# Optimization experiments

Measured on AMD Instinct MI355X. Metric: run time of the kernel, lower is better.

The kernel has to match this reference:

```python
import jax, jax.numpy as jnp
import numpy as np
from jax import lax

B, T, IN, H, OUT = 4096, 512, 2, 12, 2


def setup_inputs() -> dict:
    key = jax.random.key(0)
    ks = jax.random.split(key, 11)
    s = 1.0 / np.sqrt(H)  # PyTorch LSTM init scale
    f32 = jnp.float32
    return {
        "x": jax.random.normal(ks[0], (B, T, IN), dtype=f32),
        "W_ih0": jax.random.uniform(ks[1], (4 * H, IN), dtype=f32, minval=-s, maxval=s),
        "W_hh0": jax.random.uniform(ks[2], (4 * H, H), dtype=f32, minval=-s, maxval=s),
        "b_ih0": jax.random.uniform(ks[3], (4 * H,), dtype=f32, minval=-s, maxval=s),
        "b_hh0": jax.random.uniform(ks[4], (4 * H,), dtype=f32, minval=-s, maxval=s),
        "W_ih1": jax.random.uniform(ks[5], (4 * H, H), dtype=f32, minval=-s, maxval=s),
        "W_hh1": jax.random.uniform(ks[6], (4 * H, H), dtype=f32, minval=-s, maxval=s),
        "b_ih1": jax.random.uniform(ks[7], (4 * H,), dtype=f32, minval=-s, maxval=s),
        "b_hh1": jax.random.uniform(ks[8], (4 * H,), dtype=f32, minval=-s, maxval=s),
        "fc_W": jax.random.uniform(ks[9], (OUT, H), dtype=f32, minval=-s, maxval=s),
        "fc_b": jax.random.uniform(ks[10], (OUT,), dtype=f32, minval=-s, maxval=s),
    }


def _lstm_layer(x, W_ih, W_hh, b_ih, b_hh):
    # x: [B, T, in_dim] -> hidden trajectory [B, T, H]
    b, h = x.shape[0], W_hh.shape[1]
    # Precompute input contribution for all timesteps: [T, B, 4H]
    xg = jnp.einsum('bti,gi->tbg', x, W_ih) + b_ih + b_hh

    def step(carry, xg_t):
        hprev, cprev = carry
        gates = xg_t + hprev @ W_hh.T  # [B, 4H], PyTorch gate order i,f,g,o
        i, f, g, o = jnp.split(gates, 4, axis=-1)
        i = jax.nn.sigmoid(i)
        f = jax.nn.sigmoid(f)
        g = jnp.tanh(g)
        o = jax.nn.sigmoid(o)
        c = f * cprev + i * g
        hnew = o * jnp.tanh(c)
        return (hnew, c), hnew

    z = jnp.zeros((b, h), dtype=x.dtype)
    _, hs = lax.scan(step, (z, z), xg)  # hs: [T, B, H]
    return jnp.swapaxes(hs, 0, 1)  # [B, T, H]


def reference(x, W_ih0, W_hh0, b_ih0, b_hh0, W_ih1, W_hh1, b_ih1, b_hh1, fc_W, fc_b):
    # 2-layer LSTM, h0=c0=0; dropout is identity in eval mode.
    h1 = _lstm_layer(x, W_ih0, W_hh0, b_ih0, b_hh0)   # [B, T, H]
    h2 = _lstm_layer(h1, W_ih1, W_hh1, b_ih1, b_hh1)  # [B, T, H]
    last = h2[:, -1, :]                               # [B, H]
    return last @ fc_W.T + fc_b                       # [B, OUT]
```

## Files before the change

### kernel.cpp

```cpp
#include <hip/hip_runtime.h>


namespace {
constexpr int H  = 12;
constexpr int T  = 512;
constexpr int IN = 2;
constexpr float LOG2E = 1.4426950408889634f;

typedef float f2 __attribute__((ext_vector_type(2)));

__device__ __forceinline__ f2 pk_fma(f2 a, f2 b, f2 c) {
    f2 d;
    asm("v_pk_fma_f32 %0, %1, %2, %3" : "=v"(d) : "v"(a), "v"(b), "v"(c));
    return d;
}
__device__ __forceinline__ float exp2_(float x) {
    float r;
    asm("v_exp_f32 %0, %1" : "=v"(r) : "v"(x));
    return r;
}
__device__ __forceinline__ float rcp_(float x) { return __builtin_amdgcn_rcpf(x); }

template <int CTRL>
__device__ __forceinline__ float dppf(float v) {
    return __int_as_float(__builtin_amdgcn_update_dpp(
        __float_as_int(v), __float_as_int(v), CTRL, 0xF, 0xF, true));
}
constexpr int QP1 = 0x39;
constexpr int QP2 = 0x4E;
constexpr int QP3 = 0x93;

__device__ __forceinline__ float tanh_(float c) {
    return fmaf(2.0f, rcp_(1.0f + exp2_(-2.0f * LOG2E * c)), -1.0f);
}
}

__global__ __launch_bounds__(256, 4) void lstm2_fc_kernel(
    const float* __restrict__ x,
    const float* __restrict__ W_ih0,
    const float* __restrict__ W_hh0,
    const float* __restrict__ b_ih0,
    const float* __restrict__ b_hh0,
    const float* __restrict__ W_ih1,
    const float* __restrict__ W_hh1,
    const float* __restrict__ b_ih1,
    const float* __restrict__ b_hh1,
    const float* __restrict__ fc_W,
    const float* __restrict__ fc_b,
    float* __restrict__ out)
{
    const int lane = threadIdx.x & 63;
    const int wid  = __builtin_amdgcn_readfirstlane((int)threadIdx.x >> 6);
    const int b    = blockIdx.x * 4 + wid;
    const int u    = lane >> 2;
    const int gate = lane & 3;
    const int uc   = (u < H) ? u : 0;
    const int r    = gate * H + uc;

    const float pre  = (gate == 2) ? 2.0f : 1.0f;
    const float kmul = -LOG2E * pre;
    const float pa   = 1.0f - pre;

    __shared__ __align__(16) float sm[4 * 2 * 96];
    const int base0 = wid * 192;
    const int base1 = base0 + 96;
    const bool writer = (gate == 0) && (u < H);
    const int  woff   = writer ? uc : (16 + lane);
    const int  wslot0 = base0 + woff;
    const int  wslot1 = base1 + woff;

    f2 wx, whh0p[6], wih1p[6], whh1p[6];
    wx.x = kmul * W_ih0[r * IN + 0];
    wx.y = kmul * W_ih0[r * IN + 1];
#pragma unroll
    for (int k = 0; k < 6; ++k) {
        whh0p[k].x = kmul * W_hh0[r * H + 2 * k];
        whh0p[k].y = kmul * W_hh0[r * H + 2 * k + 1];
        wih1p[k].x = kmul * W_ih1[r * H + 2 * k];
        wih1p[k].y = kmul * W_ih1[r * H + 2 * k + 1];
        whh1p[k].x = kmul * W_hh1[r * H + 2 * k];
        whh1p[k].y = kmul * W_hh1[r * H + 2 * k + 1];
    }
    f2 bias0p, bias1p;
    bias0p.x = kmul * (b_ih0[r] + b_hh0[r]); bias0p.y = 0.0f;
    bias1p.x = kmul * (b_ih1[r] + b_hh1[r]); bias1p.y = 0.0f;

    float c0 = 0.0f, c1 = 0.0f;
    f2 hp0[6], hq1[6];
#pragma unroll
    for (int k = 0; k < 6; ++k) { hp0[k] = (f2)(0.0f); hq1[k] = (f2)(0.0f); }

    const float* xp = x + (size_t)b * T * IN;
    f2 xv; xv.x = xp[0]; xv.y = xp[1];

    for (int t = 0; t < T; ++t) {
        const int tn = (t < T - 1) ? (t + 1) : t;
        f2 xn; xn.x = xp[2 * tn + 0]; xn.y = xp[2 * tn + 1];

        f2 acc = pk_fma(wx, xv, bias0p);
#pragma unroll
        for (int k = 0; k < 6; ++k) acc = pk_fma(whh0p[k], hp0[k], acc);
        const float s0 = fmaf(pre, rcp_(1.0f + exp2_(acc.x + acc.y)), pa);
        const float f0 = dppf<QP1>(s0);
        const float g0 = dppf<QP2>(s0);
        const float o0 = dppf<QP3>(s0);
        c0 = fmaf(f0, c0, s0 * g0);
        const float h0v = o0 * tanh_(c0);
        sm[wslot0] = h0v;

        f2 accC = pk_fma(whh1p[0], hq1[0], bias1p);
#pragma unroll
        for (int k = 1; k < 6; ++k) accC = pk_fma(whh1p[k], hq1[k], accC);
#pragma unroll
        for (int k = 0; k < 6; ++k) hp0[k] = *(const f2*)&sm[base0 + 2 * k];
#pragma unroll
        for (int k = 0; k < 6; ++k) accC = pk_fma(wih1p[k], hp0[k], accC);
        const float s1 = fmaf(pre, rcp_(1.0f + exp2_(accC.x + accC.y)), pa);
        const float f1 = dppf<QP1>(s1);
        const float g1 = dppf<QP2>(s1);
        const float o1 = dppf<QP3>(s1);
        c1 = fmaf(f1, c1, s1 * g1);
        const float h1v = o1 * tanh_(c1);
        sm[wslot1] = h1v;
#pragma unroll
        for (int k = 0; k < 6; ++k) hq1[k] = *(const f2*)&sm[base1 + 2 * k];

        xv = xn;
    }

    if (lane == 0) {
        float r0 = fc_b[0];
        float r1 = fc_b[1];
#pragma unroll
        for (int k = 0; k < 6; ++k) {
            r0 = fmaf(fc_W[2 * k], hq1[k].x, r0);
            r0 = fmaf(fc_W[2 * k + 1], hq1[k].y, r0);
            r1 = fmaf(fc_W[H + 2 * k], hq1[k].x, r1);
            r1 = fmaf(fc_W[H + 2 * k + 1], hq1[k].y, r1);
        }
        float2 res; res.x = r0; res.y = r1;
        *(float2*)(out + (size_t)b * 2) = res;
    }
}

extern "C" void kernel_launch(void* const* d_in, const int* in_sizes, int n_in,
                              void* d_out, int out_size, void* d_ws, size_t ws_size,
                              hipStream_t stream) {
    const float* x     = (const float*)d_in[0];
    const float* W_ih0 = (const float*)d_in[1];
    const float* W_hh0 = (const float*)d_in[2];
    const float* b_ih0 = (const float*)d_in[3];
    const float* b_hh0 = (const float*)d_in[4];
    const float* W_ih1 = (const float*)d_in[5];
    const float* W_hh1 = (const float*)d_in[6];
    const float* b_ih1 = (const float*)d_in[7];
    const float* b_hh1 = (const float*)d_in[8];
    const float* fc_W  = (const float*)d_in[9];
    const float* fc_b  = (const float*)d_in[10];
    float* out = (float*)d_out;

    lstm2_fc_kernel<<<1024, 256, 0, stream>>>(
        x, W_ih0, W_hh0, b_ih0, b_hh0,
        W_ih1, W_hh1, b_ih1, b_hh1, fc_W, fc_b, out);
}
```

Before: 258.0 us.

## Split LSTM dot-product chains, unroll timesteps by two, load x as float4

Each gate dot product now uses three independent packed-FMA accumulators that are summed at the end, instead of one serial FMA chain. This shortens the dependency latency on the recurrent critical path. Timesteps are processed in pairs, and the two x inputs are fetched together as one float4 load. Shared-memory writes are predicated to only the writer lanes, replacing the dummy-slot trick, and compiler memory fences are added, which rely on wave-level LDS ordering for correctness.

```diff
diff --git a/kernel.cpp b/kernel.cpp
--- a/kernel.cpp
+++ b/kernel.cpp
@@ -4,22 +4,26 @@
 namespace {
 constexpr int H  = 12;
 constexpr int T  = 512;
-constexpr int IN = 2;
 constexpr float LOG2E = 1.4426950408889634f;
 
 typedef float f2 __attribute__((ext_vector_type(2)));
+typedef float f4 __attribute__((ext_vector_type(4)));
 
-__device__ __forceinline__ f2 pk_fma(f2 a, f2 b, f2 c) {
-    f2 d;
-    asm("v_pk_fma_f32 %0, %1, %2, %3" : "=v"(d) : "v"(a), "v"(b), "v"(c));
-    return d;
+__device__ __forceinline__ f2 pkfma(f2 a, f2 b, f2 c) {
+    asm("v_pk_fma_f32 %0, %1, %2, %0" : "+v"(c) : "v"(a), "v"(b));
+    return c;
+}
+__device__ __forceinline__ f2 pkmul(f2 a, f2 b) {
+    f2 d; asm("v_pk_mul_f32 %0, %1, %2" : "=v"(d) : "v"(a), "v"(b)); return d;
+}
+__device__ __forceinline__ f2 pkadd(f2 a, f2 b) {
+    f2 d; asm("v_pk_add_f32 %0, %1, %2" : "=v"(d) : "v"(a), "v"(b)); return d;
 }
 __device__ __forceinline__ float exp2_(float x) {
-    float r;
-    asm("v_exp_f32 %0, %1" : "=v"(r) : "v"(x));
-    return r;
+    float r; asm("v_exp_f32 %0, %1" : "=v"(r) : "v"(x)); return r;
 }
 __device__ __forceinline__ float rcp_(float x) { return __builtin_amdgcn_rcpf(x); }
+__device__ __forceinline__ void memfence_() { asm volatile("" ::: "memory"); }
 
 template <int CTRL>
 __device__ __forceinline__ float dppf(float v) {
@@ -29,10 +33,6 @@
 constexpr int QP1 = 0x39;
 constexpr int QP2 = 0x4E;
 constexpr int QP3 = 0x93;
-
-__device__ __forceinline__ float tanh_(float c) {
-    return fmaf(2.0f, rcp_(1.0f + exp2_(-2.0f * LOG2E * c)), -1.0f);
-}
 }
 
 __global__ __launch_bounds__(256, 4) void lstm2_fc_kernel(
@@ -60,18 +60,17 @@
     const float pre  = (gate == 2) ? 2.0f : 1.0f;
     const float kmul = -LOG2E * pre;
     const float pa   = 1.0f - pre;
+    const float km2  = -2.0f * LOG2E;
 
-    __shared__ __align__(16) float sm[4 * 2 * 96];
-    const int base0 = wid * 192;
-    const int base1 = base0 + 96;
+    __shared__ __align__(16) float sm[4 * 32];
+    float* smb = &sm[wid * 32];
     const bool writer = (gate == 0) && (u < H);
-    const int  woff   = writer ? uc : (16 + lane);
-    const int  wslot0 = base0 + woff;
-    const int  wslot1 = base1 + woff;
+    float* smw0 = smb + uc;
+    float* smw1 = smb + 16 + uc;
 
     f2 wx, whh0p[6], wih1p[6], whh1p[6];
-    wx.x = kmul * W_ih0[r * IN + 0];
-    wx.y = kmul * W_ih0[r * IN + 1];
+    wx.x = kmul * W_ih0[r * 2 + 0];
+    wx.y = kmul * W_ih0[r * 2 + 1];
 #pragma unroll
     for (int k = 0; k < 6; ++k) {
         whh0p[k].x = kmul * W_hh0[r * H + 2 * k];
@@ -90,42 +89,75 @@
 #pragma unroll
     for (int k = 0; k < 6; ++k) { hp0[k] = (f2)(0.0f); hq1[k] = (f2)(0.0f); }
 
-    const float* xp = x + (size_t)b * T * IN;
-    f2 xv; xv.x = xp[0]; xv.y = xp[1];
+    const f4* xb4 = (const f4*)(x + (size_t)b * T * 2);
+    f4 xq = xb4[0];
 
-    for (int t = 0; t < T; ++t) {
-        const int tn = (t < T - 1) ? (t + 1) : t;
-        f2 xn; xn.x = xp[2 * tn + 0]; xn.y = xp[2 * tn + 1];
+    auto step = [&](f2 xv) {
+        f2 cA = pkfma(wx, xv, bias0p);
+        cA = pkfma(whh0p[0], hp0[0], cA);
+        cA = pkfma(whh0p[1], hp0[1], cA);
+        f2 cB = pkmul(whh0p[2], hp0[2]);
+        cB = pkfma(whh0p[3], hp0[3], cB);
+        f2 cC = pkmul(whh0p[4], hp0[4]);
+        cC = pkfma(whh0p[5], hp0[5], cC);
+        cA = pkadd(cA, cB);
+        cA = pkadd(cA, cC);
+        const float s0 = fmaf(pre, rcp_(1.0f + exp2_(cA.x + cA.y)), pa);
+        const float f0v = dppf<QP1>(s0);
+        const float g0v = dppf<QP2>(s0);
+        const float o0v = dppf<QP3>(s0);
+        c0 = fmaf(f0v, c0, s0 * g0v);
+        const float h0v = o0v * fmaf(2.0f, rcp_(1.0f + exp2_(km2 * c0)), -1.0f);
+        if (writer) *smw0 = h0v;
 
-        f2 acc = pk_fma(wx, xv, bias0p);
+        f2 dA = pkfma(whh1p[0], hq1[0], bias1p);
+        dA = pkfma(whh1p[1], hq1[1], dA);
+        f2 dB = pkmul(whh1p[2], hq1[2]);
+        dB = pkfma(whh1p[3], hq1[3], dB);
+        f2 dC = pkmul(whh1p[4], hq1[4]);
+        dC = pkfma(whh1p[5], hq1[5], dC);
+        memfence_();
 #pragma unroll
-        for (int k = 0; k < 6; ++k) acc = pk_fma(whh0p[k], hp0[k], acc);
-        const float s0 = fmaf(pre, rcp_(1.0f + exp2_(acc.x + acc.y)), pa);
-        const float f0 = dppf<QP1>(s0);
-        const float g0 = dppf<QP2>(s0);
-        const float o0 = dppf<QP3>(s0);
-        c0 = fmaf(f0, c0, s0 * g0);
-        const float h0v = o0 * tanh_(c0);
-        sm[wslot0] = h0v;
+        for (int k = 0; k < 6; ++k) {
+            hp0[k].x = smb[2 * k];
+            hp0[k].y = smb[2 * k + 1];
+        }
+        dA = pkfma(wih1p[0], hp0[0], dA);
+        dA = pkfma(wih1p[1], hp0[1], dA);
+        dB = pkfma(wih1p[2], hp0[2], dB);
+        dB = pkfma(wih1p[3], hp0[3], dB);
+        dC = pkfma(wih1p[4], hp0[4], dC);
+        dC = pkfma(wih1p[5], hp0[5], dC);
+        dA = pkadd(dA, dB);
+        dA = pkadd(dA, dC);
+        const float s1 = fmaf(pre, rcp_(1.0f + exp2_(dA.x + dA.y)), pa);
+        const float f1v = dppf<QP1>(s1);
+        const float g1v = dppf<QP2>(s1);
+        const float o1v = dppf<QP3>(s1);
+        c1 = fmaf(f1v, c1, s1 * g1v);
+        const float h1v = o1v * fmaf(2.0f, rcp_(1.0f + exp2_(km2 * c1)), -1.0f);
+        if (writer) *smw1 = h1v;
+        memfence_();
+#pragma unroll
+        for (int k = 0; k < 6; ++k) {
+            hq1[k].x = smb[16 + 2 * k];
+            hq1[k].y = smb[16 + 2 * k + 1];
+        }
+    };
 
-        f2 accC = pk_fma(whh1p[0], hq1[0], bias1p);
-#pragma unroll
-        for (int k = 1; k < 6; ++k) accC = pk_fma(whh1p[k], hq1[k], accC);
-#pragma unroll
-        for (int k = 0; k < 6; ++k) hp0[k] = *(const f2*)&sm[base0 + 2 * k];
-#pragma unroll
-        for (int k = 0; k < 6; ++k) accC = pk_fma(wih1p[k], hp0[k], accC);
-        const float s1 = fmaf(pre, rcp_(1.0f + exp2_(accC.x + accC.y)), pa);
-        const float f1 = dppf<QP1>(s1);
-        const float g1 = dppf<QP2>(s1);
-        const float o1 = dppf<QP3>(s1);
-        c1 = fmaf(f1, c1, s1 * g1);
-        const float h1v = o1 * tanh_(c1);
-        sm[wslot1] = h1v;
-#pragma unroll
-        for (int k = 0; k < 6; ++k) hq1[k] = *(const f2*)&sm[base1 + 2 * k];
-
-        xv = xn;
+    for (int tt = 0; tt < T / 2 - 1; ++tt) {
+        const f4 xn = xb4[tt + 1];
+        f2 xa; xa.x = xq.x; xa.y = xq.y;
+        step(xa);
+        f2 xb; xb.x = xq.z; xb.y = xq.w;
+        step(xb);
+        xq = xn;
+    }
+    {
+        f2 xa; xa.x = xq.x; xa.y = xq.y;
+        step(xa);
+        f2 xb; xb.x = xq.z; xb.y = xq.w;
+        step(xb);
     }
 
     if (lane == 0) {
@@ -133,9 +165,9 @@
         float r1 = fc_b[1];
 #pragma unroll
         for (int k = 0; k < 6; ++k) {
-            r0 = fmaf(fc_W[2 * k], hq1[k].x, r0);
+            r0 = fmaf(fc_W[2 * k],     hq1[k].x, r0);
             r0 = fmaf(fc_W[2 * k + 1], hq1[k].y, r0);
-            r1 = fmaf(fc_W[H + 2 * k], hq1[k].x, r1);
+            r1 = fmaf(fc_W[H + 2 * k],     hq1[k].x, r1);
             r1 = fmaf(fc_W[H + 2 * k + 1], hq1[k].y, r1);
         }
         float2 res; res.x = r0; res.y = r1;
```

After: 279.6 us. 1.08x slower.
